# Performance work log

Hardware: AMD Instinct MI355X
Metric: run time of the kernel (lower is better)

Reference implementation:

```python
import jax, jax.numpy as jnp
import numpy as np
from jax import lax

Tx, Ty, NA, NS = 30, 10, 32, 64
HV, MV = 128, 64
B = 16384


def setup_inputs() -> dict:
    key = jax.random.key(0)
    ks = jax.random.split(key, 16)
    g = lambda k, s: jax.random.normal(k, s, jnp.float32) * 0.05
    return {
        "X": jax.random.normal(ks[0], (B, Tx, HV), jnp.float32),
        # pre-attention bidirectional LSTM (PyTorch gate order i,f,g,o; b = b_ih + b_hh)
        "W_ih_f": g(ks[1], (4 * NA, HV)), "W_hh_f": g(ks[2], (4 * NA, NA)), "b_f": g(ks[3], (4 * NA,)),
        "W_ih_r": g(ks[4], (4 * NA, HV)), "W_hh_r": g(ks[5], (4 * NA, NA)), "b_r": g(ks[6], (4 * NA,)),
        # attention MLP
        "W1": g(ks[7], (10, 2 * NA + NS)), "b1": g(ks[8], (10,)),
        "W2": g(ks[9], (1, 10)), "b2": g(ks[10], (1,)),
        # post-attention LSTM cell
        "W_ih_p": g(ks[11], (4 * NS, 2 * NA)), "W_hh_p": g(ks[12], (4 * NS, NS)), "b_p": g(ks[13], (4 * NS,)),
        # output projection
        "Wo": g(ks[14], (MV, NS)), "bo": g(ks[15], (MV,)),
    }


def _cell(x, h, c, W_ih, W_hh, b):
    # PyTorch LSTM cell, gate order (i, f, g, o)
    z = x @ W_ih.T + h @ W_hh.T + b
    i, f, gg, o = jnp.split(z, 4, axis=-1)
    c = jax.nn.sigmoid(f) * c + jax.nn.sigmoid(i) * jnp.tanh(gg)
    h = jax.nn.sigmoid(o) * jnp.tanh(c)
    return h, c


def _run_lstm(X, W_ih, W_hh, b):
    Bn = X.shape[0]
    H = W_hh.shape[1]
    init = (jnp.zeros((Bn, H), X.dtype), jnp.zeros((Bn, H), X.dtype))

    def step(carry, x_t):
        h, c = _cell(x_t, carry[0], carry[1], W_ih, W_hh, b)
        return (h, c), h

    _, hs = lax.scan(step, init, jnp.swapaxes(X, 0, 1))  # hs: [Tx, B, H]
    return jnp.swapaxes(hs, 0, 1)


def reference(X, W_ih_f, W_hh_f, b_f, W_ih_r, W_hh_r, b_r, W1, b1, W2, b2,
              W_ih_p, W_hh_p, b_p, Wo, bo):
    # bidirectional encoder: a is [B, Tx, 2*NA]
    a_f = _run_lstm(X, W_ih_f, W_hh_f, b_f)
    a_r = _run_lstm(X[:, ::-1, :], W_ih_r, W_hh_r, b_r)[:, ::-1, :]
    a = jnp.concatenate([a_f, a_r], axis=-1)
    Bn = X.shape[0]

    def dec_step(carry, _):
        s, c = carry
        # one_step_attention
        s_rep = jnp.broadcast_to(s[:, None, :], (Bn, Tx, NS))
        cat = jnp.concatenate([a, s_rep], axis=-1)          # [B, Tx, 2*NA+NS]
        e = jnp.tanh(cat @ W1.T + b1)                        # [B, Tx, 10]
        en = jax.nn.relu(e @ W2.T + b2)                      # [B, Tx, 1]
        alphas = jax.nn.softmax(en, axis=1)                  # softmax over Tx
        context = jnp.sum(alphas * a, axis=1)                # [B, 2*NA]
        # post-attention LSTM (single step)
        s, c = _cell(context, s, c, W_ih_p, W_hh_p, b_p)
        out = s @ Wo.T + bo                                  # [B, MV]
        return (s, c), out

    init = (jnp.zeros((Bn, NS), X.dtype), jnp.zeros((Bn, NS), X.dtype))
    _, outs = lax.scan(dec_step, init, None, length=Ty)      # [Ty, B, MV]
    return jnp.swapaxes(outs, 0, 1)                          # [B, Ty, MV]
```

## Files before the change

kernel.cpp:

```cpp
#include <hip/hip_runtime.h>

typedef unsigned short u16;
typedef unsigned int   u32;
typedef __attribute__((ext_vector_type(8))) short short8;
typedef __attribute__((ext_vector_type(4))) float f4;

#define BT 8
#define TX 30
#define TY 10

__device__ __forceinline__ float bf2f_u16(u16 h){ u32 i=((u32)h)<<16; float f; __builtin_memcpy(&f,&i,4); return f; }
__device__ __forceinline__ float lo2f(u32 p){ u32 i=p<<16; float f; __builtin_memcpy(&f,&i,4); return f; }
__device__ __forceinline__ float hi2f(u32 p){ u32 i=p&0xffff0000u; float f; __builtin_memcpy(&f,&i,4); return f; }
__device__ __forceinline__ u16 f2bf(float f){ u32 x; __builtin_memcpy(&x,&f,4); u32 r=(x+0x7fffu+((x>>16)&1u))>>16; return (u16)r; }

#if __has_builtin(__builtin_amdgcn_rcpf)
__device__ __forceinline__ float frcp(float x){ return __builtin_amdgcn_rcpf(x); }
#else
__device__ __forceinline__ float frcp(float x){ return 1.0f/x; }
#endif
__device__ __forceinline__ float sigm(float x){ return frcp(1.0f+__expf(-x)); }
__device__ __forceinline__ float tanh_(float x){ x=fminf(fmaxf(x,-15.0f),15.0f); float e=__expf(2.0f*x); return 1.0f - 2.0f*frcp(e+1.0f); }

__device__ __forceinline__ f4 mfma16(short8 a, short8 b, f4 c){
    return __builtin_amdgcn_mfma_f32_16x16x32_bf16(a, b, c, 0, 0, 0);
}

union S8u { short8 s; u32 u[4]; };

__device__ __forceinline__ void cvt_pair(float a0, float a1, u32& hp, u32& lp){
    u32 u0, u1; __builtin_memcpy(&u0,&a0,4); __builtin_memcpy(&u1,&a1,4);
    hp = __builtin_amdgcn_perm(u1, u0, 0x07060302u);
    float r0 = a0 - hi2f(u0);
    float r1 = a1 - hi2f(u1);
    u32 v0, v1; __builtin_memcpy(&v0,&r0,4); __builtin_memcpy(&v1,&r1,4);
    lp = __builtin_amdgcn_perm(v1, v0, 0x07060302u);
}

struct SDec {
    float aW1[BT][TX][10];
    u16 sh[BT][72], sl[BT][72];
    u16 ctxh[BT][72], ctxl[BT][72];
    u16 zr2[72];
    float sW1[BT][12];
    float en[BT][32];
    float w2b[12]; float b2s;
};
struct SEnc {
    u16 h[2][2][2][BT][40];
    u16 zr[40];
};
union UU { SEnc e; SDec d; };
struct Smem {
    u16 a[BT][TX][72];
    UU u;
};

__global__ __launch_bounds__(256, 2) void fused_kernel(
    const float* __restrict__ X,
    const float* __restrict__ Wihf, const float* __restrict__ Whhf, const float* __restrict__ bfv,
    const float* __restrict__ Wihr, const float* __restrict__ Whhr, const float* __restrict__ brv,
    const float* __restrict__ W1, const float* __restrict__ b1, const float* __restrict__ W2, const float* __restrict__ b2,
    const float* __restrict__ Wihp, const float* __restrict__ Whhp, const float* __restrict__ bp,
    const float* __restrict__ Wo, const float* __restrict__ bo,
    float* __restrict__ out)
{
    __shared__ __align__(16) Smem sm;
    const int tid = threadIdx.x;
    const int b0  = blockIdx.x * BT;

    {
        u32* p = (u32*)&sm.u.e;
        for (int i = tid; i < (int)(sizeof(SEnc)/4); i += 256) p[i] = 0u;
    }
    __syncthreads();

    const int lane = tid & 63;
    const int wv   = tid >> 6;
    const int mL   = lane & 15;
    const int qL   = lane >> 4;
    const int k0q  = qL * 8;
    const int ed   = wv >> 1;
    const int ub   = (wv & 1) * 16;
    const int sstep= mL >> 3;

    const float* Wih = ed ? Wihr : Wihf;
    const float* Whh = ed ? Whhr : Whhf;
    const float* bv  = ed ? brv  : bfv;

    short8 Bih[4][4]; short8 Bhh[4]; float bias4[4];
    #pragma unroll
    for (int gt = 0; gt < 4; gt++){
        const int n = gt*32 + ub + mL;
        #pragma unroll
        for (int kt = 0; kt < 4; kt++){
            const float* p = Wih + n*128 + kt*32 + k0q;
            short8 s;
            #pragma unroll
            for (int j = 0; j < 8; j++) s[j] = (short)f2bf(p[j]);
            Bih[gt][kt] = s;
        }
        {
            const float* p = Whh + n*32 + k0q;
            short8 s;
            #pragma unroll
            for (int j = 0; j < 8; j++) s[j] = (short)f2bf(p[j]);
            Bhh[gt] = s;
        }
        bias4[gt] = bv[n];
    }

    const float* xrow = X + ((long)(b0 + (mL & 7))) * TX * 128;
    float cst[4] = {0.f,0.f,0.f,0.f};

    auto epair = [&](int t, f4* cur, f4* nxt){
        if (t + 2 < TX){
            const int ts = ed ? (TX-1-(t+2+sstep)) : (t+2+sstep);
            const float* p = xrow + ts*128 + k0q;
            #pragma unroll
            for (int kt = 0; kt < 4; kt++){
                nxt[2*kt]   = *(const f4*)(p + kt*32);
                nxt[2*kt+1] = *(const f4*)(p + kt*32 + 4);
            }
        }
        const int rb = (t+1) & 1, wb = t & 1;

        f4 acc[4];
        #pragma unroll
        for (int gt = 0; gt < 4; gt++) acc[gt] = (f4){bias4[gt],bias4[gt],bias4[gt],bias4[gt]};

        #pragma unroll
        for (int kt = 0; kt < 4; kt++){
            S8u xh, xl;
            #pragma unroll
            for (int pp = 0; pp < 4; pp++){
                const f4 v = cur[2*kt + (pp>>1)];
                const int e = (pp & 1) * 2;
                cvt_pair(v[e], v[e+1], xh.u[pp], xl.u[pp]);
            }
            #pragma unroll
            for (int gt = 0; gt < 4; gt++){
                acc[gt] = mfma16(xh.s, Bih[gt][kt], acc[gt]);
                acc[gt] = mfma16(xl.s, Bih[gt][kt], acc[gt]);
            }
        }
        {
            const short8 Ahh = *(const short8*)((mL < 8) ? &sm.u.e.h[rb][ed][0][mL][k0q] : &sm.u.e.zr[k0q]);
            const short8 Ahl = *(const short8*)((mL < 8) ? &sm.u.e.h[rb][ed][1][mL][k0q] : &sm.u.e.zr[k0q]);
            #pragma unroll
            for (int gt = 0; gt < 4; gt++){
                acc[gt] = mfma16(Ahh, Bhh[gt], acc[gt]);
                acc[gt] = mfma16(Ahl, Bhh[gt], acc[gt]);
            }
        }
        if (qL < 2){
            const int tpos = ed ? (TX-1-t) : t;
            #pragma unroll
            for (int reg = 0; reg < 4; reg++){
                const int m = qL*4 + reg;
                const float ii = sigm(acc[0][reg]), ff = sigm(acc[1][reg]);
                const float gg = tanh_(acc[2][reg]), oo = sigm(acc[3][reg]);
                cst[reg] = ff*cst[reg] + ii*gg;
                const float hh = oo * tanh_(cst[reg]);
                const u16 hhi = f2bf(hh);
                const u16 hlo = f2bf(hh - bf2f_u16(hhi));
                sm.u.e.h[wb][ed][0][m][ub+mL] = hhi;
                sm.u.e.h[wb][ed][1][m][ub+mL] = hlo;
                sm.a[m][tpos][ed*32 + ub + mL] = hhi;
            }
        }
        #pragma unroll
        for (int reg = 0; reg < 4; reg++) cst[reg] = __shfl_xor(cst[reg], 32);
        __syncthreads();
        {
            const short8 Ahh = *(const short8*)((mL >= 8) ? &sm.u.e.h[wb][ed][0][mL-8][k0q] : &sm.u.e.zr[k0q]);
            const short8 Ahl = *(const short8*)((mL >= 8) ? &sm.u.e.h[wb][ed][1][mL-8][k0q] : &sm.u.e.zr[k0q]);
            #pragma unroll
            for (int gt = 0; gt < 4; gt++){
                acc[gt] = mfma16(Ahh, Bhh[gt], acc[gt]);
                acc[gt] = mfma16(Ahl, Bhh[gt], acc[gt]);
            }
        }
        if (qL >= 2){
            const int tpos = ed ? (TX-2-t) : (t+1);
            #pragma unroll
            for (int reg = 0; reg < 4; reg++){
                const int m = (qL-2)*4 + reg;
                const float ii = sigm(acc[0][reg]), ff = sigm(acc[1][reg]);
                const float gg = tanh_(acc[2][reg]), oo = sigm(acc[3][reg]);
                cst[reg] = ff*cst[reg] + ii*gg;
                const float hh = oo * tanh_(cst[reg]);
                const u16 hhi = f2bf(hh);
                const u16 hlo = f2bf(hh - bf2f_u16(hhi));
                sm.u.e.h[rb][ed][0][m][ub+mL] = hhi;
                sm.u.e.h[rb][ed][1][m][ub+mL] = hlo;
                sm.a[m][tpos][ed*32 + ub + mL] = hhi;
            }
        }
        #pragma unroll
        for (int reg = 0; reg < 4; reg++) cst[reg] = __shfl_xor(cst[reg], 32);
        __syncthreads();
    };

    f4 rawA[8], rawB[8];
    {
        const int ts0 = ed ? (TX-1-sstep) : sstep;
        const float* p = xrow + ts0*128 + k0q;
        #pragma unroll
        for (int kt = 0; kt < 4; kt++){
            rawA[2*kt]   = *(const f4*)(p + kt*32);
            rawA[2*kt+1] = *(const f4*)(p + kt*32 + 4);
        }
    }
    for (int tp = 0; tp < 28; tp += 4){ epair(tp, rawA, rawB); epair(tp+2, rawB, rawA); }
    epair(28, rawA, rawB);

    {
        u32* z = (u32*)sm.u.d.sh;
        for (int i = tid; i < (4*BT*72 + 72)/2; i += 256) z[i] = 0u;
    }
    if (tid < 10) sm.u.d.w2b[tid] = W2[tid];
    if (tid == 0) sm.u.d.b2s = b2[0];

    short8 W1aB[2][2];
    #pragma unroll
    for (int kt = 0; kt < 2; kt++){
        short8 hv8, lv8;
        #pragma unroll
        for (int j = 0; j < 8; j++){
            const float v = (mL < 10) ? W1[mL*128 + kt*32 + k0q + j] : 0.f;
            const u16 hb = f2bf(v);
            hv8[j] = (short)hb;
            lv8[j] = (short)f2bf(v - bf2f_u16(hb));
        }
        W1aB[kt][0] = hv8; W1aB[kt][1] = lv8;
    }
    const float b1v = (mL < 10) ? b1[mL] : 0.f;

    for (int tile = wv; tile < 15; tile += 4){
        f4 accA = (f4){b1v, b1v, b1v, b1v};
        const u16* abase = &sm.a[0][0][0] + (tile*16 + mL)*72;
        #pragma unroll
        for (int kt = 0; kt < 2; kt++){
            const short8 av = *(const short8*)(abase + kt*32 + k0q);
            accA = mfma16(av, W1aB[kt][0], accA);
            accA = mfma16(av, W1aB[kt][1], accA);
        }
        if (mL < 10){
            #pragma unroll
            for (int reg = 0; reg < 4; reg++){
                const int r = tile*16 + qL*4 + reg;
                (&sm.u.d.aW1[0][0][0])[r*10 + mL] = accA[reg];
            }
        }
    }

    const int uw = wv * 16;
    short8 Bip[4][2], Bhp[4][2]; float pb4[4];
    #pragma unroll
    for (int gt = 0; gt < 4; gt++){
        const int n = gt*64 + uw + mL;
        #pragma unroll
        for (int kt = 0; kt < 2; kt++){
            const float* p = Wihp + n*64 + kt*32 + k0q;
            const float* q = Whhp + n*64 + kt*32 + k0q;
            short8 s1v, s2v;
            #pragma unroll
            for (int j = 0; j < 8; j++){ s1v[j] = (short)f2bf(p[j]); s2v[j] = (short)f2bf(q[j]); }
            Bip[gt][kt] = s1v; Bhp[gt][kt] = s2v;
        }
        pb4[gt] = bp[n];
    }
    short8 Bo2[2];
    {
        const int n = uw + mL;
        #pragma unroll
        for (int kt = 0; kt < 2; kt++){
            const float* p = Wo + n*64 + kt*32 + k0q;
            short8 s;
            #pragma unroll
            for (int j = 0; j < 8; j++) s[j] = (short)f2bf(p[j]);
            Bo2[kt] = s;
        }
    }
    short8 W1sB[2];
    #pragma unroll
    for (int kt = 0; kt < 2; kt++){
        short8 s;
        #pragma unroll
        for (int j = 0; j < 8; j++){
            const float v = (mL < 10) ? W1[mL*128 + 64 + kt*32 + k0q + j] : 0.f;
            s[j] = (short)f2bf(v);
        }
        W1sB[kt] = s;
    }
    const float boL = bo[uw + mL];
    float cs2[4] = {0.f,0.f,0.f,0.f};
    __syncthreads();

    for (int ty = 0; ty < TY; ty++){
        {
            f4 accW = (f4){0.f,0.f,0.f,0.f};
            #pragma unroll
            for (int kt = 0; kt < 2; kt++){
                const int ko = kt*32 + k0q;
                const short8 shh = *(const short8*)((mL < 8) ? &sm.u.d.sh[mL][ko] : &sm.u.d.zr2[ko]);
                const short8 sll = *(const short8*)((mL < 8) ? &sm.u.d.sl[mL][ko] : &sm.u.d.zr2[ko]);
                accW = mfma16(shh, W1sB[kt], accW);
                accW = mfma16(sll, W1sB[kt], accW);
            }
            if (qL < 2 && mL < 10 && wv == 0){
                #pragma unroll
                for (int reg = 0; reg < 4; reg++) sm.u.d.sW1[qL*4+reg][mL] = accW[reg];
            }
        }
        __syncthreads();
        if (tid < 240){
            const int er = tid/30, et = tid - er*30;
            float env = sm.u.d.b2s;
            #pragma unroll
            for (int j = 0; j < 10; j++){
                const float z = sm.u.d.aW1[er][et][j] + sm.u.d.sW1[er][j];
                env += sm.u.d.w2b[j]*tanh_(z);
            }
            sm.u.d.en[er][et] = fmaxf(env, 0.f);
        }
        __syncthreads();
        {
            const int cr = tid >> 5, cup = tid & 31;
            const float* enr = sm.u.d.en[cr];
            float mx = enr[0];
            #pragma unroll
            for (int t2 = 1; t2 < TX; t2++) mx = fmaxf(mx, enr[t2]);
            float ssum = 0.f, s0 = 0.f, s1 = 0.f;
            const u16* ap = &sm.a[cr][0][2*cup];
            #pragma unroll 5
            for (int t2 = 0; t2 < TX; t2++){
                const float e = __expf(enr[t2]-mx);
                const u32 pa = *(const u32*)(ap + t2*72);
                ssum += e;
                s0 += e*lo2f(pa); s1 += e*hi2f(pa);
            }
            const float inv = frcp(ssum);
            s0 *= inv; s1 *= inv;
            const u16 h0 = f2bf(s0), h1 = f2bf(s1);
            const u16 l0 = f2bf(s0 - bf2f_u16(h0)), l1 = f2bf(s1 - bf2f_u16(h1));
            *(u32*)&sm.u.d.ctxh[cr][2*cup] = (u32)h0 | ((u32)h1 << 16);
            *(u32*)&sm.u.d.ctxl[cr][2*cup] = (u32)l0 | ((u32)l1 << 16);
        }
        __syncthreads();
        f4 acc2[4];
        #pragma unroll
        for (int gt = 0; gt < 4; gt++) acc2[gt] = (f4){pb4[gt],pb4[gt],pb4[gt],pb4[gt]};
        #pragma unroll
        for (int kt = 0; kt < 2; kt++){
            const int ko = kt*32 + k0q;
            const bool v8 = (mL < 8);
            const short8 ch  = *(const short8*)(v8 ? &sm.u.d.ctxh[mL][ko] : &sm.u.d.zr2[ko]);
            const short8 cl  = *(const short8*)(v8 ? &sm.u.d.ctxl[mL][ko] : &sm.u.d.zr2[ko]);
            const short8 shh = *(const short8*)(v8 ? &sm.u.d.sh[mL][ko]   : &sm.u.d.zr2[ko]);
            const short8 sll = *(const short8*)(v8 ? &sm.u.d.sl[mL][ko]   : &sm.u.d.zr2[ko]);
            #pragma unroll
            for (int gt = 0; gt < 4; gt++){
                acc2[gt] = mfma16(ch,  Bip[gt][kt], acc2[gt]);
                acc2[gt] = mfma16(cl,  Bip[gt][kt], acc2[gt]);
                acc2[gt] = mfma16(shh, Bhp[gt][kt], acc2[gt]);
                acc2[gt] = mfma16(sll, Bhp[gt][kt], acc2[gt]);
            }
        }
        __syncthreads();
        if (qL < 2){
            #pragma unroll
            for (int reg = 0; reg < 4; reg++){
                const int m = qL*4 + reg;
                const float ii = sigm(acc2[0][reg]), ff = sigm(acc2[1][reg]);
                const float gg = tanh_(acc2[2][reg]), oo = sigm(acc2[3][reg]);
                cs2[reg] = ff*cs2[reg] + ii*gg;
                const float sv = oo * tanh_(cs2[reg]);
                const u16 shi = f2bf(sv);
                const u16 slo = f2bf(sv - bf2f_u16(shi));
                sm.u.d.sh[m][uw+mL]  = shi;
                sm.u.d.sl[m][uw+mL]  = slo;
            }
        }
        __syncthreads();
        f4 acc3 = (f4){boL, boL, boL, boL};
        #pragma unroll
        for (int kt = 0; kt < 2; kt++){
            const int ko = kt*32 + k0q;
            const short8 shh = *(const short8*)((mL < 8) ? &sm.u.d.sh[mL][ko] : &sm.u.d.zr2[ko]);
            const short8 sll = *(const short8*)((mL < 8) ? &sm.u.d.sl[mL][ko] : &sm.u.d.zr2[ko]);
            acc3 = mfma16(shh, Bo2[kt], acc3);
            acc3 = mfma16(sll, Bo2[kt], acc3);
        }
        if (qL < 2){
            #pragma unroll
            for (int reg = 0; reg < 4; reg++){
                const int m = qL*4 + reg;
                out[(((long)(b0+m))*TY + ty)*64 + uw + mL] = acc3[reg];
            }
        }
    }
}

extern "C" void kernel_launch(void* const* d_in, const int* in_sizes, int n_in,
                              void* d_out, int out_size, void* d_ws, size_t ws_size,
                              hipStream_t stream) {
    const float* X    = (const float*)d_in[0];
    const float* Wihf = (const float*)d_in[1];
    const float* Whhf = (const float*)d_in[2];
    const float* bfv  = (const float*)d_in[3];
    const float* Wihr = (const float*)d_in[4];
    const float* Whhr = (const float*)d_in[5];
    const float* brv  = (const float*)d_in[6];
    const float* W1   = (const float*)d_in[7];
    const float* b1   = (const float*)d_in[8];
    const float* W2   = (const float*)d_in[9];
    const float* b2   = (const float*)d_in[10];
    const float* Wihp = (const float*)d_in[11];
    const float* Whhp = (const float*)d_in[12];
    const float* bp   = (const float*)d_in[13];
    const float* Wo   = (const float*)d_in[14];
    const float* bo   = (const float*)d_in[15];
    float* out = (float*)d_out;

    const int B = in_sizes[0] / (TX * 128);
    dim3 grid(B / BT), block(256);
    hipLaunchKernelGGL(fused_kernel, grid, block, 0, stream,
                       X, Wihf, Whhf, bfv, Wihr, Whhr, brv,
                       W1, b1, W2, b2, Wihp, Whhp, bp, Wo, bo, out);
}
```

Before: 637.5 us.

## Process 16 batch rows per block with swizzled LDS and fused attention scoring

Raises the per-block batch tile from 8 to 16 so every MFMA row is real work, instead of half the rows being padding or time-step pairing tricks. The encoder becomes one step per timestep without the split half-step scheme. The activation buffer drops its padding and uses an XOR-swizzled layout to avoid LDS bank conflicts. In the decoder, the precomputed a·W1 table is replaced by recomputing the full attention pre-activation each step with MFMA, and the W2 reduction is done with lane shuffles. This trades extra MFMA work and a larger LDS footprint (70KB, still two blocks per CU) for full MFMA utilization and half as many blocks.

```diff
diff --git a/kernel.cpp b/kernel.cpp
--- a/kernel.cpp
+++ b/kernel.cpp
@@ -5,7 +5,7 @@
 typedef __attribute__((ext_vector_type(8))) short short8;
 typedef __attribute__((ext_vector_type(4))) float f4;
 
-#define BT 8
+#define BT 16
 #define TX 30
 #define TY 10
 
@@ -38,23 +38,21 @@
 }
 
 struct SDec {
-    float aW1[BT][TX][10];
-    u16 sh[BT][72], sl[BT][72];
-    u16 ctxh[BT][72], ctxl[BT][72];
-    u16 zr2[72];
-    float sW1[BT][12];
-    float en[BT][32];
-    float w2b[12]; float b2s;
+    u16 sh[BT][64], sl[BT][64];
+    u16 ctxh[BT][64], ctxl[BT][64];
+    float en[BT*TX];
 };
 struct SEnc {
     u16 h[2][2][2][BT][40];
-    u16 zr[40];
 };
 union UU { SEnc e; SDec d; };
 struct Smem {
-    u16 a[BT][TX][72];
+    u16 a[BT*TX][64];
     UU u;
 };
+static_assert(sizeof(SEnc) == 10240, "enc");
+static_assert(sizeof(SDec) == 10112, "dec");
+static_assert(sizeof(Smem) == 71680, "LDS 70KB -> 2 blocks/CU");
 
 __global__ __launch_bounds__(256, 2) void fused_kernel(
     const float* __restrict__ X,
@@ -69,12 +67,6 @@
     const int tid = threadIdx.x;
     const int b0  = blockIdx.x * BT;
 
-    {
-        u32* p = (u32*)&sm.u.e;
-        for (int i = tid; i < (int)(sizeof(SEnc)/4); i += 256) p[i] = 0u;
-    }
-    __syncthreads();
-
     const int lane = tid & 63;
     const int wv   = tid >> 6;
     const int mL   = lane & 15;
@@ -82,7 +74,12 @@
     const int k0q  = qL * 8;
     const int ed   = wv >> 1;
     const int ub   = (wv & 1) * 16;
-    const int sstep= mL >> 3;
+
+    {
+        u32* p = (u32*)&sm.u.e;
+        for (int i = tid; i < 2560; i += 256) p[i] = 0u;
+    }
+    __syncthreads();
 
     const float* Wih = ed ? Wihr : Wihf;
     const float* Whh = ed ? Whhr : Whhf;
@@ -110,12 +107,12 @@
         bias4[gt] = bv[n];
     }
 
-    const float* xrow = X + ((long)(b0 + (mL & 7))) * TX * 128;
+    const float* xrow = X + ((long)(b0 + mL)) * TX * 128;
     float cst[4] = {0.f,0.f,0.f,0.f};
 
-    auto epair = [&](int t, f4* cur, f4* nxt){
-        if (t + 2 < TX){
-            const int ts = ed ? (TX-1-(t+2+sstep)) : (t+2+sstep);
+    auto estep = [&](int t, f4* cur, f4* nxt){
+        if (t + 1 < TX){
+            const int ts = ed ? (TX-2-t) : (t+1);
             const float* p = xrow + ts*128 + k0q;
             #pragma unroll
             for (int kt = 0; kt < 4; kt++){
@@ -132,12 +129,10 @@
         #pragma unroll
         for (int kt = 0; kt < 4; kt++){
             S8u xh, xl;
-            #pragma unroll
-            for (int pp = 0; pp < 4; pp++){
-                const f4 v = cur[2*kt + (pp>>1)];
-                const int e = (pp & 1) * 2;
-                cvt_pair(v[e], v[e+1], xh.u[pp], xl.u[pp]);
-            }
+            cvt_pair(cur[2*kt][0],   cur[2*kt][1],   xh.u[0], xl.u[0]);
+            cvt_pair(cur[2*kt][2],   cur[2*kt][3],   xh.u[1], xl.u[1]);
+            cvt_pair(cur[2*kt+1][0], cur[2*kt+1][1], xh.u[2], xl.u[2]);
+            cvt_pair(cur[2*kt+1][2], cur[2*kt+1][3], xh.u[3], xl.u[3]);
             #pragma unroll
             for (int gt = 0; gt < 4; gt++){
                 acc[gt] = mfma16(xh.s, Bih[gt][kt], acc[gt]);
@@ -145,66 +140,36 @@
             }
         }
         {
-            const short8 Ahh = *(const short8*)((mL < 8) ? &sm.u.e.h[rb][ed][0][mL][k0q] : &sm.u.e.zr[k0q]);
-            const short8 Ahl = *(const short8*)((mL < 8) ? &sm.u.e.h[rb][ed][1][mL][k0q] : &sm.u.e.zr[k0q]);
+            const short8 Ahh = *(const short8*)&sm.u.e.h[rb][ed][0][mL][k0q];
+            const short8 Ahl = *(const short8*)&sm.u.e.h[rb][ed][1][mL][k0q];
             #pragma unroll
             for (int gt = 0; gt < 4; gt++){
                 acc[gt] = mfma16(Ahh, Bhh[gt], acc[gt]);
                 acc[gt] = mfma16(Ahl, Bhh[gt], acc[gt]);
             }
         }
-        if (qL < 2){
-            const int tpos = ed ? (TX-1-t) : t;
-            #pragma unroll
-            for (int reg = 0; reg < 4; reg++){
-                const int m = qL*4 + reg;
-                const float ii = sigm(acc[0][reg]), ff = sigm(acc[1][reg]);
-                const float gg = tanh_(acc[2][reg]), oo = sigm(acc[3][reg]);
-                cst[reg] = ff*cst[reg] + ii*gg;
-                const float hh = oo * tanh_(cst[reg]);
-                const u16 hhi = f2bf(hh);
-                const u16 hlo = f2bf(hh - bf2f_u16(hhi));
-                sm.u.e.h[wb][ed][0][m][ub+mL] = hhi;
-                sm.u.e.h[wb][ed][1][m][ub+mL] = hlo;
-                sm.a[m][tpos][ed*32 + ub + mL] = hhi;
-            }
-        }
-        #pragma unroll
-        for (int reg = 0; reg < 4; reg++) cst[reg] = __shfl_xor(cst[reg], 32);
-        __syncthreads();
-        {
-            const short8 Ahh = *(const short8*)((mL >= 8) ? &sm.u.e.h[wb][ed][0][mL-8][k0q] : &sm.u.e.zr[k0q]);
-            const short8 Ahl = *(const short8*)((mL >= 8) ? &sm.u.e.h[wb][ed][1][mL-8][k0q] : &sm.u.e.zr[k0q]);
-            #pragma unroll
-            for (int gt = 0; gt < 4; gt++){
-                acc[gt] = mfma16(Ahh, Bhh[gt], acc[gt]);
-                acc[gt] = mfma16(Ahl, Bhh[gt], acc[gt]);
-            }
-        }
-        if (qL >= 2){
-            const int tpos = ed ? (TX-2-t) : (t+1);
-            #pragma unroll
-            for (int reg = 0; reg < 4; reg++){
-                const int m = (qL-2)*4 + reg;
-                const float ii = sigm(acc[0][reg]), ff = sigm(acc[1][reg]);
-                const float gg = tanh_(acc[2][reg]), oo = sigm(acc[3][reg]);
-                cst[reg] = ff*cst[reg] + ii*gg;
-                const float hh = oo * tanh_(cst[reg]);
-                const u16 hhi = f2bf(hh);
-                const u16 hlo = f2bf(hh - bf2f_u16(hhi));
-                sm.u.e.h[rb][ed][0][m][ub+mL] = hhi;
-                sm.u.e.h[rb][ed][1][m][ub+mL] = hlo;
-                sm.a[m][tpos][ed*32 + ub + mL] = hhi;
-            }
-        }
-        #pragma unroll
-        for (int reg = 0; reg < 4; reg++) cst[reg] = __shfl_xor(cst[reg], 32);
+        const int tpos = ed ? (TX-1-t) : t;
+        const int u = ed*32 + ub + mL;
+        #pragma unroll
+        for (int reg = 0; reg < 4; reg++){
+            const int m = qL*4 + reg;
+            const float ii = sigm(acc[0][reg]), ff = sigm(acc[1][reg]);
+            const float gg = tanh_(acc[2][reg]), oo = sigm(acc[3][reg]);
+            cst[reg] = ff*cst[reg] + ii*gg;
+            const float hh = oo * tanh_(cst[reg]);
+            const u16 hhi = f2bf(hh);
+            const u16 hlo = f2bf(hh - bf2f_u16(hhi));
+            sm.u.e.h[wb][ed][0][m][ub+mL] = hhi;
+            sm.u.e.h[wb][ed][1][m][ub+mL] = hlo;
+            const int r = m*TX + tpos;
+            sm.a[r][(((u>>3) ^ ((m+tpos)&7))<<3) | (u&7)] = hhi;
+        }
         __syncthreads();
     };
 
     f4 rawA[8], rawB[8];
     {
-        const int ts0 = ed ? (TX-1-sstep) : sstep;
+        const int ts0 = ed ? (TX-1) : 0;
         const float* p = xrow + ts0*128 + k0q;
         #pragma unroll
         for (int kt = 0; kt < 4; kt++){
@@ -212,16 +177,12 @@
             rawA[2*kt+1] = *(const f4*)(p + kt*32 + 4);
         }
     }
-    for (int tp = 0; tp < 28; tp += 4){ epair(tp, rawA, rawB); epair(tp+2, rawB, rawA); }
-    epair(28, rawA, rawB);
+    for (int t = 0; t < TX; t += 2){ estep(t, rawA, rawB); estep(t+1, rawB, rawA); }
 
     {
         u32* z = (u32*)sm.u.d.sh;
-        for (int i = tid; i < (4*BT*72 + 72)/2; i += 256) z[i] = 0u;
-    }
-    if (tid < 10) sm.u.d.w2b[tid] = W2[tid];
-    if (tid == 0) sm.u.d.b2s = b2[0];
-
+        for (int i = tid; i < 1024; i += 256) z[i] = 0u;
+    }
     short8 W1aB[2][2];
     #pragma unroll
     for (int kt = 0; kt < 2; kt++){
@@ -235,25 +196,20 @@
         }
         W1aB[kt][0] = hv8; W1aB[kt][1] = lv8;
     }
+    short8 W1sB[2];
+    #pragma unroll
+    for (int kt = 0; kt < 2; kt++){
+        short8 s;
+        #pragma unroll
+        for (int j = 0; j < 8; j++){
+            const float v = (mL < 10) ? W1[mL*128 + 64 + kt*32 + k0q + j] : 0.f;
+            s[j] = (short)f2bf(v);
+        }
+        W1sB[kt] = s;
+    }
     const float b1v = (mL < 10) ? b1[mL] : 0.f;
-
-    for (int tile = wv; tile < 15; tile += 4){
-        f4 accA = (f4){b1v, b1v, b1v, b1v};
-        const u16* abase = &sm.a[0][0][0] + (tile*16 + mL)*72;
-        #pragma unroll
-        for (int kt = 0; kt < 2; kt++){
-            const short8 av = *(const short8*)(abase + kt*32 + k0q);
-            accA = mfma16(av, W1aB[kt][0], accA);
-            accA = mfma16(av, W1aB[kt][1], accA);
-        }
-        if (mL < 10){
-            #pragma unroll
-            for (int reg = 0; reg < 4; reg++){
-                const int r = tile*16 + qL*4 + reg;
-                (&sm.u.d.aW1[0][0][0])[r*10 + mL] = accA[reg];
-            }
-        }
-    }
+    const float w2v = (mL < 10) ? W2[mL] : 0.f;
+    const float b2s = b2[0];
 
     const int uw = wv * 16;
     short8 Bip[4][2], Bhp[4][2]; float pb4[4];
@@ -283,70 +239,82 @@
             Bo2[kt] = s;
         }
     }
-    short8 W1sB[2];
-    #pragma unroll
-    for (int kt = 0; kt < 2; kt++){
-        short8 s;
-        #pragma unroll
-        for (int j = 0; j < 8; j++){
-            const float v = (mL < 10) ? W1[mL*128 + 64 + kt*32 + k0q + j] : 0.f;
-            s[j] = (short)f2bf(v);
-        }
-        W1sB[kt] = s;
-    }
     const float boL = bo[uw + mL];
     float cs2[4] = {0.f,0.f,0.f,0.f};
+    const u16* aflat  = &sm.a[0][0];
+    u16* shf = &sm.u.d.sh[0][0];
+    u16* slf = &sm.u.d.sl[0][0];
+    u16* chf = &sm.u.d.ctxh[0][0];
+    u16* clf = &sm.u.d.ctxl[0][0];
     __syncthreads();
 
     for (int ty = 0; ty < TY; ty++){
+        for (int tt = wv; tt < TX; tt += 4){
+            const int r = tt*16 + mL;
+            const int b = (r * 34953) >> 20;
+            const int tp2 = r - b*30;
+            f4 accE = (f4){b1v, b1v, b1v, b1v};
+            const u16* ab = aflat + r*64;
+            const int keyA = (b + tp2) & 7;
+            #pragma unroll
+            for (int kt = 0; kt < 2; kt++){
+                const short8 av = *(const short8*)(ab + (((kt*4+qL)^keyA)<<3));
+                accE = mfma16(av, W1aB[kt][0], accE);
+                accE = mfma16(av, W1aB[kt][1], accE);
+            }
+            const int keyS = b & 7;
+            #pragma unroll
+            for (int kt = 0; kt < 2; kt++){
+                const int off = b*64 + (((kt*4+qL)^keyS)<<3);
+                const short8 shh = *(const short8*)(shf + off);
+                const short8 sll = *(const short8*)(slf + off);
+                accE = mfma16(shh, W1sB[kt], accE);
+                accE = mfma16(sll, W1sB[kt], accE);
+            }
+            float er[4];
+            #pragma unroll
+            for (int reg = 0; reg < 4; reg++) er[reg] = w2v * tanh_(accE[reg]);
+            #pragma unroll
+            for (int d = 1; d < 16; d <<= 1){
+                #pragma unroll
+                for (int reg = 0; reg < 4; reg++) er[reg] += __shfl_xor(er[reg], d);
+            }
+            if (mL == 0){
+                f4 ev;
+                #pragma unroll
+                for (int reg = 0; reg < 4; reg++) ev[reg] = fmaxf(er[reg] + b2s, 0.f);
+                *(f4*)&sm.u.d.en[tt*16 + qL*4] = ev;
+            }
+        }
+        __syncthreads();
         {
-            f4 accW = (f4){0.f,0.f,0.f,0.f};
-            #pragma unroll
-            for (int kt = 0; kt < 2; kt++){
-                const int ko = kt*32 + k0q;
-                const short8 shh = *(const short8*)((mL < 8) ? &sm.u.d.sh[mL][ko] : &sm.u.d.zr2[ko]);
-                const short8 sll = *(const short8*)((mL < 8) ? &sm.u.d.sl[mL][ko] : &sm.u.d.zr2[ko]);
-                accW = mfma16(shh, W1sB[kt], accW);
-                accW = mfma16(sll, W1sB[kt], accW);
-            }
-            if (qL < 2 && mL < 10 && wv == 0){
-                #pragma unroll
-                for (int reg = 0; reg < 4; reg++) sm.u.d.sW1[qL*4+reg][mL] = accW[reg];
-            }
-        }
-        __syncthreads();
-        if (tid < 240){
-            const int er = tid/30, et = tid - er*30;
-            float env = sm.u.d.b2s;
-            #pragma unroll
-            for (int j = 0; j < 10; j++){
-                const float z = sm.u.d.aW1[er][et][j] + sm.u.d.sW1[er][j];
-                env += sm.u.d.w2b[j]*tanh_(z);
-            }
-            sm.u.d.en[er][et] = fmaxf(env, 0.f);
-        }
-        __syncthreads();
-        {
-            const int cr = tid >> 5, cup = tid & 31;
-            const float* enr = sm.u.d.en[cr];
+            const int cr = tid >> 4, cup = tid & 15;
+            const float* enr = &sm.u.d.en[cr*30];
             float mx = enr[0];
             #pragma unroll
             for (int t2 = 1; t2 < TX; t2++) mx = fmaxf(mx, enr[t2]);
-            float ssum = 0.f, s0 = 0.f, s1 = 0.f;
-            const u16* ap = &sm.a[cr][0][2*cup];
+            float ssum = 0.f, s0 = 0.f, s1 = 0.f, s2v_ = 0.f, s3 = 0.f;
             #pragma unroll 5
             for (int t2 = 0; t2 < TX; t2++){
                 const float e = __expf(enr[t2]-mx);
-                const u32 pa = *(const u32*)(ap + t2*72);
+                const u16* ap = aflat + (cr*30+t2)*64
+                              + ((((cup>>1) ^ ((cr+t2)&7))<<3) | ((cup&1)<<2));
+                const u32 pa0 = *(const u32*)ap;
+                const u32 pa1 = *(const u32*)(ap + 2);
                 ssum += e;
-                s0 += e*lo2f(pa); s1 += e*hi2f(pa);
+                s0 += e*lo2f(pa0); s1 += e*hi2f(pa0);
+                s2v_ += e*lo2f(pa1); s3 += e*hi2f(pa1);
             }
             const float inv = frcp(ssum);
-            s0 *= inv; s1 *= inv;
-            const u16 h0 = f2bf(s0), h1 = f2bf(s1);
+            s0 *= inv; s1 *= inv; s2v_ *= inv; s3 *= inv;
+            const u16 h0 = f2bf(s0), h1 = f2bf(s1), h2 = f2bf(s2v_), h3 = f2bf(s3);
             const u16 l0 = f2bf(s0 - bf2f_u16(h0)), l1 = f2bf(s1 - bf2f_u16(h1));
-            *(u32*)&sm.u.d.ctxh[cr][2*cup] = (u32)h0 | ((u32)h1 << 16);
-            *(u32*)&sm.u.d.ctxl[cr][2*cup] = (u32)l0 | ((u32)l1 << 16);
+            const u16 l2 = f2bf(s2v_ - bf2f_u16(h2)), l3 = f2bf(s3 - bf2f_u16(h3));
+            const int off = cr*64 + ((((cup>>1) ^ (cr&7))<<3) | ((cup&1)<<2));
+            *(u32*)(chf + off)     = (u32)h0 | ((u32)h1 << 16);
+            *(u32*)(chf + off + 2) = (u32)h2 | ((u32)h3 << 16);
+            *(u32*)(clf + off)     = (u32)l0 | ((u32)l1 << 16);
+            *(u32*)(clf + off + 2) = (u32)l2 | ((u32)l3 << 16);
         }
         __syncthreads();
         f4 acc2[4];
@@ -354,12 +322,11 @@
         for (int gt = 0; gt < 4; gt++) acc2[gt] = (f4){pb4[gt],pb4[gt],pb4[gt],pb4[gt]};
         #pragma unroll
         for (int kt = 0; kt < 2; kt++){
-            const int ko = kt*32 + k0q;
-            const bool v8 = (mL < 8);
-            const short8 ch  = *(const short8*)(v8 ? &sm.u.d.ctxh[mL][ko] : &sm.u.d.zr2[ko]);
-            const short8 cl  = *(const short8*)(v8 ? &sm.u.d.ctxl[mL][ko] : &sm.u.d.zr2[ko]);
-            const short8 shh = *(const short8*)(v8 ? &sm.u.d.sh[mL][ko]   : &sm.u.d.zr2[ko]);
-            const short8 sll = *(const short8*)(v8 ? &sm.u.d.sl[mL][ko]   : &sm.u.d.zr2[ko]);
+            const int off = mL*64 + (((kt*4+qL) ^ (mL&7))<<3);
+            const short8 ch  = *(const short8*)(chf + off);
+            const short8 cl  = *(const short8*)(clf + off);
+            const short8 shh = *(const short8*)(shf + off);
+            const short8 sll = *(const short8*)(slf + off);
             #pragma unroll
             for (int gt = 0; gt < 4; gt++){
                 acc2[gt] = mfma16(ch,  Bip[gt][kt], acc2[gt]);
@@ -369,36 +336,34 @@
             }
         }
         __syncthreads();
-        if (qL < 2){
-            #pragma unroll
-            for (int reg = 0; reg < 4; reg++){
-                const int m = qL*4 + reg;
-                const float ii = sigm(acc2[0][reg]), ff = sigm(acc2[1][reg]);
-                const float gg = tanh_(acc2[2][reg]), oo = sigm(acc2[3][reg]);
-                cs2[reg] = ff*cs2[reg] + ii*gg;
-                const float sv = oo * tanh_(cs2[reg]);
-                const u16 shi = f2bf(sv);
-                const u16 slo = f2bf(sv - bf2f_u16(shi));
-                sm.u.d.sh[m][uw+mL]  = shi;
-                sm.u.d.sl[m][uw+mL]  = slo;
-            }
+        #pragma unroll
+        for (int reg = 0; reg < 4; reg++){
+            const int m = qL*4 + reg;
+            const float ii = sigm(acc2[0][reg]), ff = sigm(acc2[1][reg]);
+            const float gg = tanh_(acc2[2][reg]), oo = sigm(acc2[3][reg]);
+            cs2[reg] = ff*cs2[reg] + ii*gg;
+            const float sv = oo * tanh_(cs2[reg]);
+            const u16 shi = f2bf(sv);
+            const u16 slo = f2bf(sv - bf2f_u16(shi));
+            const int u2 = uw + mL;
+            const int idx = m*64 + ((((u2>>3) ^ (m&7))<<3) | (u2&7));
+            shf[idx] = shi;
+            slf[idx] = slo;
         }
         __syncthreads();
         f4 acc3 = (f4){boL, boL, boL, boL};
         #pragma unroll
         for (int kt = 0; kt < 2; kt++){
-            const int ko = kt*32 + k0q;
-            const short8 shh = *(const short8*)((mL < 8) ? &sm.u.d.sh[mL][ko] : &sm.u.d.zr2[ko]);
-            const short8 sll = *(const short8*)((mL < 8) ? &sm.u.d.sl[mL][ko] : &sm.u.d.zr2[ko]);
+            const int off = mL*64 + (((kt*4+qL) ^ (mL&7))<<3);
+            const short8 shh = *(const short8*)(shf + off);
+            const short8 sll = *(const short8*)(slf + off);
             acc3 = mfma16(shh, Bo2[kt], acc3);
             acc3 = mfma16(sll, Bo2[kt], acc3);
         }
-        if (qL < 2){
-            #pragma unroll
-            for (int reg = 0; reg < 4; reg++){
-                const int m = qL*4 + reg;
-                out[(((long)(b0+m))*TY + ty)*64 + uw + mL] = acc3[reg];
-            }
+        #pragma unroll
+        for (int reg = 0; reg < 4; reg++){
+            const int m = qL*4 + reg;
+            out[(((long)(b0+m))*TY + ty)*64 + uw + mL] = acc3[reg];
         }
     }
 }
```

Measured after the change: 614.6 us. -3.6%, faster.
